# Performance work log

Measured on AMD Instinct MI355X. Metric: run time of the kernel, lower is better.

## Reference

```python
import jax, jax.numpy as jnp
import numpy as np

EMBED_DIM = 1024
NUM_HEADS = 16
HEAD_DIM = EMBED_DIM // NUM_HEADS


def setup_inputs() -> dict:
    key = jax.random.key(0)
    ks = jax.random.split(key, 11)
    B, T, C = 2, 2048, EMBED_DIM
    s = 1.0 / np.sqrt(C)  # ~ torch Linear init scale
    inp = {
        "q": jax.random.normal(ks[0], (B, T, C), jnp.float32),
        "k": jax.random.normal(ks[1], (B, T, C), jnp.float32),
        "v": jax.random.normal(ks[2], (B, T, C), jnp.float32),
        "Wq": jax.random.normal(ks[3], (C, C), jnp.float32) * s,
        "bq": jax.random.normal(ks[4], (C,), jnp.float32) * s,
        "Wk": jax.random.normal(ks[5], (C, C), jnp.float32) * s,
        "bk": jax.random.normal(ks[6], (C,), jnp.float32) * s,
        "Wv": jax.random.normal(ks[7], (C, C), jnp.float32) * s,
        "bv": jax.random.normal(ks[8], (C,), jnp.float32) * s,
        "Wo": jax.random.normal(ks[9], (C, C), jnp.float32) * s,
        "bo": jax.random.normal(ks[10], (C,), jnp.float32) * s,
    }
    return inp


def _split_heads(x):
    B, T, C = x.shape
    return x.reshape(B, T, NUM_HEADS, HEAD_DIM).transpose(0, 2, 1, 3)  # [B,H,T,Dh]


def reference(q, k, v, Wq, bq, Wk, bk, Wv, bv, Wo, bo):
    B, Tq, C = q.shape
    # torch Linear: y = x @ W.T + b
    qh = _split_heads(q @ Wq.T + bq)
    kh = _split_heads(k @ Wk.T + bk)
    vh = _split_heads(v @ Wv.T + bv)
    scale = 1.0 / np.sqrt(HEAD_DIM).astype(np.float32)
    logits = jnp.einsum("bhqd,bhkd->bhqk", qh, kh) * scale
    attn = jax.nn.softmax(logits, axis=-1)
    out = jnp.einsum("bhqk,bhkd->bhqd", attn, vh)
    out = out.transpose(0, 2, 1, 3).reshape(B, Tq, C)
    return out @ Wo.T + bo
```

## Files before the change

### kernel.cpp

```cpp
#include <hip/hip_runtime.h>
#include <stdint.h>

#define T_SEQ 2048
#define CDIM 1024
#define NHEAD 16
#define HDIM 64
#define MROWS 4096

typedef unsigned short u16;
typedef __attribute__((ext_vector_type(8))) short bf16x8;
typedef __attribute__((ext_vector_type(4))) float f32x4;
typedef __attribute__((ext_vector_type(4))) unsigned short u16x4;

#if __has_builtin(__builtin_amdgcn_exp2f)
#define EXP2(x) __builtin_amdgcn_exp2f(x)
#else
#define EXP2(x) exp2f(x)
#endif

__device__ __forceinline__ u16 f2bf(float f) {
  unsigned u = __builtin_bit_cast(unsigned, f);
  u += 0x7fffu + ((u >> 16) & 1u);
  return (u16)(u >> 16);
}

__device__ __forceinline__ unsigned cvt_pk_bf16(float lo, float hi) {
  unsigned r;
  asm("v_cvt_pk_bf16_f32 %0, %1, %2" : "=v"(r) : "v"(lo), "v"(hi));
  return r;
}

__device__ __forceinline__ void gll16(const void* g, void* l) {
  __builtin_amdgcn_global_load_lds((__attribute__((address_space(1))) void*)(g),
                                   (__attribute__((address_space(3))) void*)(l),
                                   16, 0, 0);
}

__global__ __launch_bounds__(256)
void cvt_all(const float* __restrict__ q, const float* __restrict__ k, const float* __restrict__ v,
             const float* __restrict__ wq, const float* __restrict__ wk,
             const float* __restrict__ wv, const float* __restrict__ wo,
             u16* __restrict__ qb, u16* __restrict__ kb, u16* __restrict__ vb,
             u16* __restrict__ wqb, u16* __restrict__ wkb, u16* __restrict__ wvb, u16* __restrict__ wob) {
  int b = blockIdx.x;
  const float* src; u16* dst; int base;
  if (b < 1536) {
    int s = b >> 9;
    src = (s == 0) ? q : (s == 1) ? k : v;
    dst = (s == 0) ? qb : (s == 1) ? kb : vb;
    base = (b & 511) * 2048;
  } else {
    int s = (b - 1536) >> 7;
    src = (s == 0) ? wq : (s == 1) ? wk : (s == 2) ? wv : wo;
    dst = (s == 0) ? wqb : (s == 1) ? wkb : (s == 2) ? wvb : wob;
    base = ((b - 1536) & 127) * 2048;
  }
#pragma unroll
  for (int j = 0; j < 8; ++j) {
    int i = base + j * 256 + threadIdx.x;
    float4 a = ((const float4*)src)[i];
    u16x4 o = { f2bf(a.x), f2bf(a.y), f2bf(a.z), f2bf(a.w) };
    ((u16x4*)dst)[i] = o;
  }
}


__device__ __forceinline__ void gemm_stage(const u16* Ag, const u16* Bg, u16* Ad, u16* Bd) {
#pragma unroll
  for (int c = 0; c < 4; ++c) {
    gll16(Ag + c * 32 * CDIM, Ad + c * 2048);
    gll16(Bg + c * 32 * CDIM, Bd + c * 2048);
  }
}

__device__ __forceinline__ void gemm_compute(const u16* As, const u16* Bs,
                                             f32x4 (&acc)[4][4],
                                             int wr, int wc, int lg, int lr) {
#pragma unroll
  for (int kk = 0; kk < 2; ++kk) {
    bf16x8 af[4], bfr[4];
#pragma unroll
    for (int f = 0; f < 4; ++f) {
      int ra = wr * 64 + f * 16 + lr;
      af[f]  = *(const bf16x8*)((const char*)As + ra * 128 + ((lg * 16 + kk * 64) ^ ((ra & 7) << 4)));
      int rb = wc * 64 + f * 16 + lr;
      bfr[f] = *(const bf16x8*)((const char*)Bs + rb * 128 + ((lg * 16 + kk * 64) ^ ((rb & 7) << 4)));
    }
#pragma unroll
    for (int i = 0; i < 4; ++i)
#pragma unroll
      for (int j = 0; j < 4; ++j)
        acc[i][j] = __builtin_amdgcn_mfma_f32_16x16x32_bf16(af[i], bfr[j], acc[i][j], 0, 0, 0);
  }
}

__global__ __launch_bounds__(256)
void gemm_qkv(const u16* __restrict__ A0, const u16* __restrict__ A1, const u16* __restrict__ A2,
              const u16* __restrict__ W0, const u16* __restrict__ W1, const u16* __restrict__ W2,
              const float* __restrict__ b0, const float* __restrict__ b1, const float* __restrict__ b2,
              u16* __restrict__ o0, u16* __restrict__ o1, u16* __restrict__ o2,
              float qscale) {
  __shared__ u16 As[2][128 * 64];
  __shared__ u16 Bs[2][128 * 64];
  const int z = blockIdx.z;
  const u16* A   = (z == 0) ? A0 : (z == 1) ? A1 : A2;
  const u16* Bw  = (z == 0) ? W0 : (z == 1) ? W1 : W2;
  const float* bias = (z == 0) ? b0 : (z == 1) ? b1 : b2;
  u16* outp = (z == 0) ? o0 : (z == 1) ? o1 : o2;
  const float scale = (z == 0) ? qscale : 1.0f;

  const int m0 = blockIdx.y * 128;
  const int n0 = blockIdx.x * 128;
  const int tid = threadIdx.x;
  const int w = tid >> 6, l = tid & 63;
  const int wr = w >> 1, wc = w & 1;
  const int lg = l >> 4, lr = l & 15;

  const int row0 = tid >> 3, slot0 = tid & 7;
  const int so = (slot0 ^ (row0 & 7)) << 3;
  const u16* Ag = A  + ((size_t)(m0 + row0)) * CDIM + so;
  const u16* Bg = Bw + ((size_t)(n0 + row0)) * CDIM + so;
  u16* Ad0 = As[0] + w * 512;  u16* Bd0 = Bs[0] + w * 512;
  u16* Ad1 = As[1] + w * 512;  u16* Bd1 = Bs[1] + w * 512;

  f32x4 acc[4][4] = {};

  gemm_stage(Ag, Bg, Ad0, Bd0);
  __syncthreads();
#pragma unroll 1
  for (int kt = 0; kt < 16; kt += 2) {
    gemm_stage(Ag + (kt + 1) * 64, Bg + (kt + 1) * 64, Ad1, Bd1);
    gemm_compute(As[0], Bs[0], acc, wr, wc, lg, lr);
    __syncthreads();
    if (kt + 2 < 16)
      gemm_stage(Ag + (kt + 2) * 64, Bg + (kt + 2) * 64, Ad0, Bd0);
    gemm_compute(As[1], Bs[1], acc, wr, wc, lg, lr);
    __syncthreads();
  }

#pragma unroll
  for (int fj = 0; fj < 4; ++fj) {
    int col = n0 + wc * 64 + fj * 16 + lr;
    float bv = bias[col];
    int h = col >> 6, d = col & 63;
#pragma unroll
    for (int fi = 0; fi < 4; ++fi) {
#pragma unroll
      for (int i = 0; i < 4; ++i) {
        int row = m0 + wr * 64 + fi * 16 + lg * 4 + i;
        float val = (acc[fi][fj][i] + bv) * scale;
        int b = row >> 11, t = row & 2047;
        if (z < 2)
          outp[(((size_t)(b * NHEAD + h)) * T_SEQ + t) * HDIM + d] = f2bf(val);
        else
          outp[(((size_t)(b * NHEAD + h)) * HDIM + d) * T_SEQ + t] = f2bf(val);
      }
    }
  }
}

__global__ __launch_bounds__(256)
void gemm_bt0(const u16* __restrict__ A, const u16* __restrict__ Bw,
              const float* __restrict__ bias, float* __restrict__ outp) {
  __shared__ u16 As[2][128 * 64];
  __shared__ u16 Bs[2][128 * 64];
  const int m0 = blockIdx.y * 128;
  const int n0 = blockIdx.x * 128;
  const int tid = threadIdx.x;
  const int w = tid >> 6, l = tid & 63;
  const int wr = w >> 1, wc = w & 1;
  const int lg = l >> 4, lr = l & 15;

  const int row0 = tid >> 3, slot0 = tid & 7;
  const int so = (slot0 ^ (row0 & 7)) << 3;
  const u16* Ag = A  + ((size_t)(m0 + row0)) * CDIM + so;
  const u16* Bg = Bw + ((size_t)(n0 + row0)) * CDIM + so;
  u16* Ad0 = As[0] + w * 512;  u16* Bd0 = Bs[0] + w * 512;
  u16* Ad1 = As[1] + w * 512;  u16* Bd1 = Bs[1] + w * 512;

  f32x4 acc[4][4] = {};

  gemm_stage(Ag, Bg, Ad0, Bd0);
  __syncthreads();
#pragma unroll 1
  for (int kt = 0; kt < 16; kt += 2) {
    gemm_stage(Ag + (kt + 1) * 64, Bg + (kt + 1) * 64, Ad1, Bd1);
    gemm_compute(As[0], Bs[0], acc, wr, wc, lg, lr);
    __syncthreads();
    if (kt + 2 < 16)
      gemm_stage(Ag + (kt + 2) * 64, Bg + (kt + 2) * 64, Ad0, Bd0);
    gemm_compute(As[1], Bs[1], acc, wr, wc, lg, lr);
    __syncthreads();
  }

#pragma unroll
  for (int fj = 0; fj < 4; ++fj) {
    int col = n0 + wc * 64 + fj * 16 + lr;
    float bv = bias[col];
#pragma unroll
    for (int fi = 0; fi < 4; ++fi) {
#pragma unroll
      for (int i = 0; i < 4; ++i) {
        int row = m0 + wr * 64 + fi * 16 + lg * 4 + i;
        outp[(size_t)row * CDIM + col] = acc[fi][fj][i] + bv;
      }
    }
  }
}


__device__ __forceinline__ void attn_stage(const u16* Kg, const u16* Vg, u16* Kd, u16* Vd) {
#pragma unroll
  for (int c = 0; c < 2; ++c) {
    gll16(Kg + c * 32 * HDIM,  Kd + c * 2048);
    gll16(Vg + c * 32 * T_SEQ, Vd + c * 2048);
  }
}

__device__ __forceinline__ void attn_process(const u16* Ks, const u16* Vs, u16* pw,
                                             bf16x8 qf0, bf16x8 qf1,
                                             f32x4 (&acc)[4], f32x4& lsum, float& m_run,
                                             int lg, int lr) {
  f32x4 s[4] = {};
  __builtin_amdgcn_s_setprio(1);
#pragma unroll
  for (int kk = 0; kk < 2; ++kk) {
    bf16x8 qf = kk ? qf1 : qf0;
#pragma unroll
    for (int fn = 0; fn < 4; ++fn) {
      int r = fn * 16 + lr;
      bf16x8 kf = *(const bf16x8*)((const char*)Ks + r * 128 + ((lg * 16 + kk * 64) ^ ((r & 7) << 4)));
      s[fn] = __builtin_amdgcn_mfma_f32_16x16x32_bf16(kf, qf, s[fn], 0, 0, 0);
    }
  }
  __builtin_amdgcn_s_setprio(0);

  float a0 = fmaxf(fmaxf(s[0][0], s[0][1]), s[0][2]);
  float a1 = fmaxf(fmaxf(s[0][3], s[1][0]), s[1][1]);
  float a2 = fmaxf(fmaxf(s[1][2], s[1][3]), s[2][0]);
  float a3 = fmaxf(fmaxf(s[2][1], s[2][2]), s[2][3]);
  float a4 = fmaxf(fmaxf(s[3][0], s[3][1]), s[3][2]);
  float tmax = fmaxf(fmaxf(fmaxf(a0, a1), fmaxf(a2, a3)), fmaxf(a4, s[3][3]));
  tmax = fmaxf(tmax, __shfl_xor(tmax, 16));
  tmax = fmaxf(tmax, __shfl_xor(tmax, 32));

  if (!__all(tmax <= m_run + 8.f)) {
    float m_new = fmaxf(m_run, tmax);
    float alpha = EXP2(m_run - m_new);
    lsum[0] *= alpha; lsum[1] *= alpha; lsum[2] *= alpha; lsum[3] *= alpha;
#pragma unroll
    for (int fd = 0; fd < 4; ++fd) {
      acc[fd][0] *= alpha; acc[fd][1] *= alpha;
      acc[fd][2] *= alpha; acc[fd][3] *= alpha;
    }
    m_run = m_new;
  }

#pragma unroll
  for (int fn = 0; fn < 4; ++fn) {
    float p0 = EXP2(s[fn][0] - m_run);
    float p1 = EXP2(s[fn][1] - m_run);
    float p2 = EXP2(s[fn][2] - m_run);
    float p3 = EXP2(s[fn][3] - m_run);
    lsum[fn] += (p0 + p1) + (p2 + p3);
    uint2 pk;
    pk.x = cvt_pk_bf16(p0, p1);
    pk.y = cvt_pk_bf16(p2, p3);
    *(uint2*)((char*)pw + lr * 128 + ((fn * 32 + lg * 8) ^ ((lr & 7) << 4))) = pk;
  }

#pragma unroll
  for (int kk = 0; kk < 2; ++kk) {
    bf16x8 pf = *(const bf16x8*)((const char*)pw + lr * 128 + ((lg * 16 + kk * 64) ^ ((lr & 7) << 4)));
    __builtin_amdgcn_s_setprio(1);
#pragma unroll
    for (int fd = 0; fd < 4; ++fd) {
      int r = fd * 16 + lr;
      bf16x8 vf = *(const bf16x8*)((const char*)Vs + r * 128 + ((lg * 16 + kk * 64) ^ ((r & 7) << 4)));
      acc[fd] = __builtin_amdgcn_mfma_f32_16x16x32_bf16(vf, pf, acc[fd], 0, 0, 0);
    }
    __builtin_amdgcn_s_setprio(0);
  }
}

__global__ __launch_bounds__(256)
void attn_fused(const u16* __restrict__ Qh, const u16* __restrict__ Kh,
                const u16* __restrict__ Vt, u16* __restrict__ Ao) {
  __shared__ u16 Ks[2][64 * 64];
  __shared__ u16 Vs[2][64 * 64];
  __shared__ u16 Ps[4][16 * 64];
  const int bh = blockIdx.y;
  const int q0 = blockIdx.x * 64;
  const int tid = threadIdx.x;
  const int w = tid >> 6, l = tid & 63;
  const int lg = l >> 4, lr = l & 15;

  const u16* qptr = Qh + ((size_t)bh * T_SEQ + q0 + w * 16 + lr) * HDIM + lg * 8;
  bf16x8 qf0 = *(const bf16x8*)qptr;
  bf16x8 qf1 = *(const bf16x8*)(qptr + 32);

  const int row0 = tid >> 3, slot0 = tid & 7;
  const int so = (slot0 ^ (row0 & 7)) << 3;
  const u16* Kg = Kh + ((size_t)bh * T_SEQ + row0) * HDIM + so;
  const u16* Vg = Vt + ((size_t)bh * HDIM + row0) * T_SEQ + so;
  u16* Kd0 = Ks[0] + w * 512;  u16* Vd0 = Vs[0] + w * 512;
  u16* Kd1 = Ks[1] + w * 512;  u16* Vd1 = Vs[1] + w * 512;

  f32x4 acc[4] = {};
  f32x4 lsum = {};
  float m_run = -1e30f;
  u16* pw = Ps[w];

  attn_stage(Kg, Vg, Kd0, Vd0);
  __syncthreads();
#pragma unroll 1
  for (int kv = 0; kv < 32; kv += 2) {
    attn_stage(Kg + (size_t)(kv + 1) * 64 * HDIM, Vg + (kv + 1) * 64, Kd1, Vd1);
    attn_process(Ks[0], Vs[0], pw, qf0, qf1, acc, lsum, m_run, lg, lr);
    __syncthreads();
    if (kv + 2 < 32)
      attn_stage(Kg + (size_t)(kv + 2) * 64 * HDIM, Vg + (kv + 2) * 64, Kd0, Vd0);
    attn_process(Ks[1], Vs[1], pw, qf0, qf1, acc, lsum, m_run, lg, lr);
    __syncthreads();
  }

  float lr_sum = (lsum[0] + lsum[1]) + (lsum[2] + lsum[3]);
  lr_sum += __shfl_xor(lr_sum, 16);
  lr_sum += __shfl_xor(lr_sum, 32);
  float inv = 1.f / lr_sum;

  int b = bh >> 4, h = bh & 15;
  u16* orow = Ao + ((size_t)(b * T_SEQ + q0 + w * 16 + lr)) * CDIM + h * HDIM;
#pragma unroll
  for (int fd = 0; fd < 4; ++fd) {
    uint2 ov;
    ov.x = cvt_pk_bf16(acc[fd][0] * inv, acc[fd][1] * inv);
    ov.y = cvt_pk_bf16(acc[fd][2] * inv, acc[fd][3] * inv);
    *(uint2*)(orow + fd * 16 + lg * 4) = ov;
  }
}

extern "C" void kernel_launch(void* const* d_in, const int* in_sizes, int n_in,
                              void* d_out, int out_size, void* d_ws, size_t ws_size,
                              hipStream_t stream) {
  const float* q  = (const float*)d_in[0];
  const float* k  = (const float*)d_in[1];
  const float* v  = (const float*)d_in[2];
  const float* Wq = (const float*)d_in[3];
  const float* bq = (const float*)d_in[4];
  const float* Wk = (const float*)d_in[5];
  const float* bk = (const float*)d_in[6];
  const float* Wv = (const float*)d_in[7];
  const float* bv = (const float*)d_in[8];
  const float* Wo = (const float*)d_in[9];
  const float* bo = (const float*)d_in[10];

  char* ws = (char*)d_ws;
  size_t off = 0;
  auto alloc = [&](size_t n) { void* p = ws + off; off += (n + 255) & ~(size_t)255; return p; };
  const size_t NX = (size_t)MROWS * CDIM;
  const size_t NW = (size_t)CDIM * CDIM;
  u16* qb  = (u16*)alloc(NX * 2);
  u16* kb  = (u16*)alloc(NX * 2);
  u16* vb  = (u16*)alloc(NX * 2);
  u16* Wqb = (u16*)alloc(NW * 2);
  u16* Wkb = (u16*)alloc(NW * 2);
  u16* Wvb = (u16*)alloc(NW * 2);
  u16* Wob = (u16*)alloc(NW * 2);
  u16* Qhp = (u16*)alloc(NX * 2);
  u16* Khp = (u16*)alloc(NX * 2);
  u16* Vtp = (u16*)alloc(NX * 2);
  u16* Aop = (u16*)alloc(NX * 2);

  cvt_all<<<2048, 256, 0, stream>>>(q, k, v, Wq, Wk, Wv, Wo,
                                    qb, kb, vb, Wqb, Wkb, Wvb, Wob);

  const float qscale = 0.18033688011112042f;
  gemm_qkv<<<dim3(CDIM / 128, MROWS / 128, 3), 256, 0, stream>>>(
      qb, kb, vb, Wqb, Wkb, Wvb, bq, bk, bv, Qhp, Khp, Vtp, qscale);

  attn_fused<<<dim3(T_SEQ / 64, 32), 256, 0, stream>>>(Qhp, Khp, Vtp, Aop);

  gemm_bt0<<<dim3(CDIM / 128, MROWS / 128), 256, 0, stream>>>(Aop, Wob, bo, (float*)d_out);

  (void)in_sizes; (void)n_in; (void)out_size; (void)ws_size;
}
```

Measured before the change: 155.8 us.

## Use partial vmcnt waits with raw barriers to overlap prefetch in GEMM and attention

Replaces __syncthreads-based double buffering in both GEMM kernels and the attention loop with explicit s_barrier plus s_waitcnt vmcnt(N). The next tile's global-to-LDS loads can then stay in flight while the current tile is consumed, instead of draining all outstanding memory ops at each sync. The last iteration issues a redundant load of the final tile to keep the wait count uniform, which adds some extra memory traffic. It also moves the cross-lane max shuffles inside the rare rescale branch so the common path skips them. That relies on the per-lane threshold check remaining valid, and the hand-tuned wait counts must match the actual number of loads issued per stage.

```diff
diff --git a/kernel.cpp b/kernel.cpp
--- a/kernel.cpp
+++ b/kernel.cpp
@@ -35,6 +35,15 @@
                                    (__attribute__((address_space(3))) void*)(l),
                                    16, 0, 0);
 }
+
+__device__ __forceinline__ void wg_barrier() {
+  asm volatile("" ::: "memory");
+  __builtin_amdgcn_s_barrier();
+  asm volatile("" ::: "memory");
+}
+
+#define WAIT_VM(N) do { __builtin_amdgcn_s_waitcnt(0xF00 | 0x70 | (N)); \
+                        asm volatile("" ::: "memory"); } while (0)
 
 __global__ __launch_bounds__(256)
 void cvt_all(const float* __restrict__ q, const float* __restrict__ k, const float* __restrict__ v,
@@ -94,6 +103,20 @@
   }
 }
 
+#define GEMM_KLOOP(As, Bs, Ad0, Bd0, Ad1, Bd1)                                 \
+  gemm_stage(Ag, Bg, Ad0, Bd0);                                                \
+  _Pragma("unroll 1")                                                          \
+  for (int kt = 0; kt < 16; ++kt) {                                            \
+    wg_barrier();                                                              \
+    int nt = (kt + 1 < 16) ? kt + 1 : 15;                                      \
+    if (kt & 1) gemm_stage(Ag + nt * 64, Bg + nt * 64, Ad0, Bd0);              \
+    else        gemm_stage(Ag + nt * 64, Bg + nt * 64, Ad1, Bd1);              \
+    WAIT_VM(8);                                                                \
+    wg_barrier();                                                              \
+    gemm_compute((kt & 1) ? As[1] : As[0], (kt & 1) ? Bs[1] : Bs[0],           \
+                 acc, wr, wc, lg, lr);                                         \
+  }
+
 __global__ __launch_bounds__(256)
 void gemm_qkv(const u16* __restrict__ A0, const u16* __restrict__ A1, const u16* __restrict__ A2,
               const u16* __restrict__ W0, const u16* __restrict__ W1, const u16* __restrict__ W2,
@@ -125,18 +148,7 @@
 
   f32x4 acc[4][4] = {};
 
-  gemm_stage(Ag, Bg, Ad0, Bd0);
-  __syncthreads();
-#pragma unroll 1
-  for (int kt = 0; kt < 16; kt += 2) {
-    gemm_stage(Ag + (kt + 1) * 64, Bg + (kt + 1) * 64, Ad1, Bd1);
-    gemm_compute(As[0], Bs[0], acc, wr, wc, lg, lr);
-    __syncthreads();
-    if (kt + 2 < 16)
-      gemm_stage(Ag + (kt + 2) * 64, Bg + (kt + 2) * 64, Ad0, Bd0);
-    gemm_compute(As[1], Bs[1], acc, wr, wc, lg, lr);
-    __syncthreads();
-  }
+  GEMM_KLOOP(As, Bs, Ad0, Bd0, Ad1, Bd1)
 
 #pragma unroll
   for (int fj = 0; fj < 4; ++fj) {
@@ -180,18 +192,7 @@
 
   f32x4 acc[4][4] = {};
 
-  gemm_stage(Ag, Bg, Ad0, Bd0);
-  __syncthreads();
-#pragma unroll 1
-  for (int kt = 0; kt < 16; kt += 2) {
-    gemm_stage(Ag + (kt + 1) * 64, Bg + (kt + 1) * 64, Ad1, Bd1);
-    gemm_compute(As[0], Bs[0], acc, wr, wc, lg, lr);
-    __syncthreads();
-    if (kt + 2 < 16)
-      gemm_stage(Ag + (kt + 2) * 64, Bg + (kt + 2) * 64, Ad0, Bd0);
-    gemm_compute(As[1], Bs[1], acc, wr, wc, lg, lr);
-    __syncthreads();
-  }
+  GEMM_KLOOP(As, Bs, Ad0, Bd0, Ad1, Bd1)
 
 #pragma unroll
   for (int fj = 0; fj < 4; ++fj) {
@@ -235,16 +236,14 @@
   }
   __builtin_amdgcn_s_setprio(0);
 
-  float a0 = fmaxf(fmaxf(s[0][0], s[0][1]), s[0][2]);
-  float a1 = fmaxf(fmaxf(s[0][3], s[1][0]), s[1][1]);
-  float a2 = fmaxf(fmaxf(s[1][2], s[1][3]), s[2][0]);
-  float a3 = fmaxf(fmaxf(s[2][1], s[2][2]), s[2][3]);
-  float a4 = fmaxf(fmaxf(s[3][0], s[3][1]), s[3][2]);
-  float tmax = fmaxf(fmaxf(fmaxf(a0, a1), fmaxf(a2, a3)), fmaxf(a4, s[3][3]));
-  tmax = fmaxf(tmax, __shfl_xor(tmax, 16));
-  tmax = fmaxf(tmax, __shfl_xor(tmax, 32));
-
-  if (!__all(tmax <= m_run + 8.f)) {
+  float t0 = fmaxf(fmaxf(s[0][0], s[0][1]), fmaxf(s[0][2], s[0][3]));
+  float t1 = fmaxf(fmaxf(s[1][0], s[1][1]), fmaxf(s[1][2], s[1][3]));
+  float t2 = fmaxf(fmaxf(s[2][0], s[2][1]), fmaxf(s[2][2], s[2][3]));
+  float t3 = fmaxf(fmaxf(s[3][0], s[3][1]), fmaxf(s[3][2], s[3][3]));
+  float tl = fmaxf(fmaxf(t0, t1), fmaxf(t2, t3));
+  if (!__all(tl <= m_run + 8.f)) {
+    float tmax = fmaxf(tl, __shfl_xor(tl, 16));
+    tmax = fmaxf(tmax, __shfl_xor(tmax, 32));
     float m_new = fmaxf(m_run, tmax);
     float alpha = EXP2(m_run - m_new);
     lsum[0] *= alpha; lsum[1] *= alpha; lsum[2] *= alpha; lsum[3] *= alpha;
@@ -312,16 +311,16 @@
   u16* pw = Ps[w];
 
   attn_stage(Kg, Vg, Kd0, Vd0);
-  __syncthreads();
 #pragma unroll 1
-  for (int kv = 0; kv < 32; kv += 2) {
-    attn_stage(Kg + (size_t)(kv + 1) * 64 * HDIM, Vg + (kv + 1) * 64, Kd1, Vd1);
-    attn_process(Ks[0], Vs[0], pw, qf0, qf1, acc, lsum, m_run, lg, lr);
-    __syncthreads();
-    if (kv + 2 < 32)
-      attn_stage(Kg + (size_t)(kv + 2) * 64 * HDIM, Vg + (kv + 2) * 64, Kd0, Vd0);
-    attn_process(Ks[1], Vs[1], pw, qf0, qf1, acc, lsum, m_run, lg, lr);
-    __syncthreads();
+  for (int kv = 0; kv < 32; ++kv) {
+    wg_barrier();
+    int nt = (kv + 1 < 32) ? kv + 1 : 31;
+    if (kv & 1) attn_stage(Kg + (size_t)nt * 64 * HDIM, Vg + nt * 64, Kd0, Vd0);
+    else        attn_stage(Kg + (size_t)nt * 64 * HDIM, Vg + nt * 64, Kd1, Vd1);
+    WAIT_VM(4);
+    wg_barrier();
+    attn_process((kv & 1) ? Ks[1] : Ks[0], (kv & 1) ? Vs[1] : Vs[0],
+                 pw, qf0, qf1, acc, lsum, m_run, lg, lr);
   }
 
   float lr_sum = (lsum[0] + lsum[1]) + (lsum[2] + lsum[3]);
```

Result: faster. 140.7 us (-9.7%).
